# Kernel optimization log

Hardware: AMD Instinct MI355X
Metric: run time of the kernel (lower is better)

The kernel has to match this reference:

```python
import jax, jax.numpy as jnp
import numpy as np

REL_SIZE = 65
TAG_SIZE = 4


def _rope(y):
    # Interleaved rotary position embedding, matching the torch module:
    # cos_pos = cos(theta) repeat_interleave(2), sin_pos = sin(theta) repeat_interleave(2)
    # y2 = (-y1, y0, -y3, y2, ...)
    B, S, H = y.shape
    half = H // 2
    pos = jnp.arange(S, dtype=jnp.float32)[:, None]                      # (S,1)
    inv_freq = jnp.power(10000.0, -2.0 * jnp.arange(half, dtype=jnp.float32) / H)
    theta = pos * inv_freq                                               # (S, half)
    cos = jnp.repeat(jnp.cos(theta), 2, axis=-1)                          # (S, H)
    sin = jnp.repeat(jnp.sin(theta), 2, axis=-1)                          # (S, H)
    yr = y.reshape(B, S, half, 2)
    y2 = jnp.stack([-yr[..., 1], yr[..., 0]], axis=-1).reshape(B, S, H)
    return y * cos + y2 * sin


def setup_inputs() -> dict:
    key = jax.random.key(0)
    k1, k2, k3 = jax.random.split(key, 3)
    B, S, H = 1, 160, 768
    y = jax.random.normal(k1, (B, S, H), dtype=jnp.float32)
    event_idx = jax.random.randint(k2, (B, 16), 0, S)
    W1 = jax.random.normal(k3, (H, 2 * H), dtype=jnp.float32) * 0.02
    b1 = jnp.zeros((H,), dtype=jnp.float32)
    W2 = jax.random.normal(jax.random.fold_in(key, 7), (REL_SIZE * TAG_SIZE, H), dtype=jnp.float32) * 0.02
    b2 = jnp.zeros((REL_SIZE * TAG_SIZE,), dtype=jnp.float32)
    return {"y": y, "event_idx": event_idx, "W1": W1, "b1": b1, "W2": W2, "b2": b2}


def reference(y, event_idx, W1, b1, W2, b2):
    # Eval path (training=False): event_idx unused, dropout = identity, sigmoid applied.
    B, S, H = y.shape
    yrot = _rope(y)
    # Linear(cat(a, b)) is separable: split W1 into the halves acting on a and b.
    Wa, Wb = W1[:, :H], W1[:, H:]
    left = jnp.einsum('bsh,oh->bso', yrot, Wa)                  # contribution of token i (row)
    right = jnp.einsum('bsh,oh->bso', yrot, Wb) + b1            # contribution of token j (col)
    h = jax.nn.relu(left[:, :, None, :] + right[:, None, :, :])  # (B, S, S, H)
    out = jnp.einsum('bijh,oh->bijo', h, W2) + b2               # (B, S, S, 260)
    out = out.reshape(B, S, S, REL_SIZE, TAG_SIZE).transpose(0, 3, 1, 2, 4)  # (B, 65, S, S, 4)
    return jax.nn.sigmoid(out)
```

## Files before the change

### kernel.cpp

```cpp
#include <hip/hip_runtime.h>
#include <hip/hip_bf16.h>
#include <cstdint>

#define SDIM 160
#define HDIM 768
#define HALF 384
#define ODIM 260
#define OPAD 272
#define CHUNK_BYTES 34816
#define WS_SMALL 1155088
#define WS_BIG   3514384

typedef __attribute__((ext_vector_type(8))) short short8;
typedef __attribute__((ext_vector_type(4))) float floatx4;

static __device__ __forceinline__ float bf2f(unsigned short u) {
    union { unsigned int i; float f; } v; v.i = ((unsigned int)u) << 16; return v.f;
}
static __device__ __forceinline__ unsigned short f2bf(float x) {
    __hip_bfloat16 h = __float2bfloat16(x);
    return *reinterpret_cast<unsigned short*>(&h);
}
static __device__ __forceinline__ float q(float x) { return bf2f(f2bf(x)); }

__global__ __launch_bounds__(256) void prep_kernel(
    const float* __restrict__ y, const float* __restrict__ W1,
    const float* __restrict__ W2,
    unsigned short* __restrict__ yb, unsigned short* __restrict__ W2b,
    unsigned short* __restrict__ W1b) {
    int bid = blockIdx.x;
    int t = threadIdx.x;
    if (bid < SDIM) {
        int s = bid;
        for (int p = t; p < HALF; p += 256) {
            float invf = __expf(-(2.0f * (float)p / (float)HDIM) * 9.210340371976184f);
            float th = (float)s * invf;
            float c = cosf(th), sn = sinf(th);
            float y0 = y[s * HDIM + 2 * p], y1 = y[s * HDIM + 2 * p + 1];
            yb[s * HDIM + 2 * p]     = f2bf(y0 * c - y1 * sn);
            yb[s * HDIM + 2 * p + 1] = f2bf(y1 * c + y0 * sn);
        }
    } else if (bid < SDIM + 816) {
        int idx = (bid - SDIM) * 256 + t;
        int kg = idx / (OPAD * 8);
        int rem = idx - kg * (OPAD * 8);
        int row = rem >> 3, e = rem & 7;
        W2b[idx] = (row < ODIM) ? f2bf(W2[row * HDIM + kg * 8 + e])
                                : (unsigned short)0;
    } else {
        int idx = (bid - SDIM - 816) * 256 + t;
        int kg = idx / 12288;
        int rem = idx - kg * 12288;
        int row = rem >> 3, e = rem & 7;
        float v = (row < 768) ? W1[row * 1536 + kg * 8 + e]
                              : W1[(row - 768) * 1536 + 768 + kg * 8 + e];
        W1b[idx] = f2bf(v);
    }
}

__global__ __launch_bounds__(64, 2) void lr3_kernel(
    const unsigned short* __restrict__ yb, const unsigned short* __restrict__ W1b,
    const float* __restrict__ b1,
    unsigned short* __restrict__ Lb, unsigned short* __restrict__ Rb) {
    int l = threadIdx.x & 63;
    int l16 = l & 15, qd = l >> 4;
    int mtb = blockIdx.x * 4;
    int sp = blockIdx.y;
    int s0 = sp * 32 + l16;
    int s1 = s0 + 16;

    floatx4 acc[2][4];
    #pragma unroll
    for (int st = 0; st < 2; ++st)
        #pragma unroll
        for (int mtl = 0; mtl < 4; ++mtl)
            acc[st][mtl] = (floatx4){0.0f, 0.0f, 0.0f, 0.0f};

    const unsigned short* yrow0 = yb + s0 * HDIM;
    const unsigned short* yrow1 = yb + s1 * HDIM;

    for (int ks = 0; ks < 24; ++ks) {
        int k = ks * 32 + qd * 8;
        int kg = ks * 4 + qd;
        union { uint4 u; short8 s; } bu0, bu1;
        bu0.u = *reinterpret_cast<const uint4*>(yrow0 + k);
        bu1.u = *reinterpret_cast<const uint4*>(yrow1 + k);
        #pragma unroll
        for (int mtl = 0; mtl < 4; ++mtl) {
            union { uint4 u; short8 s; } au;
            au.u = *reinterpret_cast<const uint4*>(
                W1b + ((size_t)kg * 1536 + (mtb + mtl) * 16 + l16) * 8);
            acc[0][mtl] = __builtin_amdgcn_mfma_f32_16x16x32_bf16(
                au.s, bu0.s, acc[0][mtl], 0, 0, 0);
            acc[1][mtl] = __builtin_amdgcn_mfma_f32_16x16x32_bf16(
                au.s, bu1.s, acc[1][mtl], 0, 0, 0);
        }
    }

    #pragma unroll
    for (int st = 0; st < 2; ++st) {
        int s_out = sp * 32 + st * 16 + l16;
        #pragma unroll
        for (int mtl = 0; mtl < 4; ++mtl) {
            int o2 = (mtb + mtl) * 16 + qd * 4;
            unsigned short out4[4];
            if (o2 < 768) {
                #pragma unroll
                for (int r = 0; r < 4; ++r) out4[r] = f2bf(acc[st][mtl][r]);
                *reinterpret_cast<uint2*>(Lb + s_out * HDIM + o2) =
                    *reinterpret_cast<uint2*>(out4);
            } else {
                int ob = o2 - 768;
                #pragma unroll
                for (int r = 0; r < 4; ++r)
                    out4[r] = f2bf(acc[st][mtl][r] + b1[ob + r]);
                *reinterpret_cast<uint2*>(Rb + s_out * HDIM + ob) =
                    *reinterpret_cast<uint2*>(out4);
            }
        }
    }
}

__global__ __launch_bounds__(256) void lr_fallback_kernel(
    const unsigned short* __restrict__ yb, const float* __restrict__ W1,
    const float* __restrict__ b1,
    unsigned short* __restrict__ Lb, unsigned short* __restrict__ Rb) {
    int idx = blockIdx.x * 256 + threadIdx.x;
    int s = idx / 1536;
    int o2 = idx - s * 1536;
    const unsigned short* yrow = yb + s * HDIM;
    if (o2 < 768) {
        const float* wp = W1 + o2 * 1536;
        float a0 = 0.0f;
        for (int k = 0; k < HDIM; ++k) a0 += q(wp[k]) * bf2f(yrow[k]);
        Lb[s * HDIM + o2] = f2bf(a0);
    } else {
        int ob = o2 - 768;
        const float* wp = W1 + ob * 1536 + 768;
        float a0 = 0.0f;
        for (int k = 0; k < HDIM; ++k) a0 += q(wp[k]) * bf2f(yrow[k]);
        Rb[s * HDIM + ob] = f2bf(a0 + b1[ob]);
    }
}

__global__ __launch_bounds__(128, 3) void main_kernel(
    const unsigned short* __restrict__ Lb, const unsigned short* __restrict__ Rb,
    const unsigned short* __restrict__ W2b,
    const float* __restrict__ b2, float* __restrict__ out) {
    __shared__ __align__(16) unsigned char lds[CHUNK_BYTES];

    int w = threadIdx.x >> 6;
    int l = threadIdx.x & 63;
    int l16 = l & 15, qd = l >> 4;
    int mt0 = w * 9;
    int nmt = w ? 8 : 9;
    int i0 = blockIdx.x * 2;
    int j0 = blockIdx.y * 16;
    int j = j0 + l16;

    floatx4 acc[2][9];
    #pragma unroll
    for (int c = 0; c < 2; ++c)
        #pragma unroll
        for (int mtl = 0; mtl < 9; ++mtl)
            acc[c][mtl] = (floatx4){0.0f, 0.0f, 0.0f, 0.0f};

    const unsigned short* Lrow0 = Lb + i0 * HDIM;
    const unsigned short* Lrow1 = Lb + (i0 + 1) * HDIM;
    const unsigned short* Rrow  = Rb + j * HDIM;

    for (int kc = 0; kc < 12; ++kc) {
        __syncthreads();
        const uint4* gsrc = reinterpret_cast<const uint4*>(
            reinterpret_cast<const unsigned char*>(W2b) + kc * CHUNK_BYTES);
        uint4* ldsv = reinterpret_cast<uint4*>(lds);
        #pragma unroll
        for (int it = 0; it < 17; ++it) {
            int idx = it * 128 + threadIdx.x;
            ldsv[idx] = gsrc[idx];
        }
        __syncthreads();
        #pragma unroll
        for (int ks = 0; ks < 2; ++ks) {
            int k = kc * 64 + ks * 32 + qd * 8;
            short8 bfrag[2];
            #pragma unroll
            for (int c = 0; c < 2; ++c) {
                const unsigned short* Lr = c ? Lrow1 : Lrow0;
                union { uint4 u; unsigned short us[8]; } lu, ru;
                lu.u = *reinterpret_cast<const uint4*>(Lr + k);
                ru.u = *reinterpret_cast<const uint4*>(Rrow + k);
                short8 hb;
                #pragma unroll
                for (int e = 0; e < 8; ++e) {
                    float hv = bf2f(lu.us[e]) + bf2f(ru.us[e]);
                    hb[e] = (short)f2bf(fmaxf(hv, 0.0f));
                }
                bfrag[c] = hb;
            }
            int ldsbase = ((ks * 4 + qd) * OPAD + l16) * 16;
            #pragma unroll
            for (int mtl = 0; mtl < 9; ++mtl) {
                if (mtl < nmt) {
                    union { uint4 u; short8 s; } au;
                    au.u = *reinterpret_cast<const uint4*>(
                        lds + ldsbase + (mt0 + mtl) * 256);
                    acc[0][mtl] = __builtin_amdgcn_mfma_f32_16x16x32_bf16(
                        au.s, bfrag[0], acc[0][mtl], 0, 0, 0);
                    acc[1][mtl] = __builtin_amdgcn_mfma_f32_16x16x32_bf16(
                        au.s, bfrag[1], acc[1][mtl], 0, 0, 0);
                }
            }
        }
    }

    #pragma unroll
    for (int c = 0; c < 2; ++c) {
        int i = i0 + c;
        #pragma unroll
        for (int mtl = 0; mtl < 9; ++mtl) {
            if (mtl < nmt) {
                int ob = (mt0 + mtl) * 16 + qd * 4;
                if (ob < ODIM) {
                    float4 bv = *reinterpret_cast<const float4*>(b2 + ob);
                    int rel = ob >> 2;
                    float4 v;
                    v.x = 1.0f / (1.0f + __expf(-(acc[c][mtl][0] + bv.x)));
                    v.y = 1.0f / (1.0f + __expf(-(acc[c][mtl][1] + bv.y)));
                    v.z = 1.0f / (1.0f + __expf(-(acc[c][mtl][2] + bv.z)));
                    v.w = 1.0f / (1.0f + __expf(-(acc[c][mtl][3] + bv.w)));
                    *reinterpret_cast<float4*>(
                        out + (((rel * SDIM) + i) * SDIM + j) * 4) = v;
                }
            }
        }
    }
}

__global__ void ws_too_small_kernel(float* out) { out[0] = 999.0f; }

extern "C" void kernel_launch(void* const* d_in, const int* in_sizes, int n_in,
                              void* d_out, int out_size, void* d_ws, size_t ws_size,
                              hipStream_t stream) {
    const float* y  = (const float*)d_in[0];
    const float* W1 = (const float*)d_in[2];
    const float* b1 = (const float*)d_in[3];
    const float* W2 = (const float*)d_in[4];
    const float* b2 = (const float*)d_in[5];
    float* out = (float*)d_out;

    if (ws_size < (size_t)WS_SMALL) {
        ws_too_small_kernel<<<dim3(1), dim3(1), 0, stream>>>(out);
        return;
    }

    unsigned short* yb  = (unsigned short*)((char*)d_ws + 16);
    unsigned short* Lb  = yb + SDIM * HDIM;
    unsigned short* Rb  = Lb + SDIM * HDIM;
    unsigned short* W2b = Rb + SDIM * HDIM;
    unsigned short* W1b = W2b + 96 * OPAD * 8;

    if (ws_size >= (size_t)WS_BIG) {
        prep_kernel<<<dim3(SDIM + 816 + 4608), dim3(256), 0, stream>>>(
            y, W1, W2, yb, W2b, W1b);
        lr3_kernel<<<dim3(24, 5), dim3(64), 0, stream>>>(yb, W1b, b1, Lb, Rb);
        main_kernel<<<dim3(80, 10), dim3(128), 0, stream>>>(Lb, Rb, W2b, b2, out);
    } else {
        prep_kernel<<<dim3(SDIM + 816), dim3(256), 0, stream>>>(
            y, W1, W2, yb, W2b, W1b);
        lr_fallback_kernel<<<dim3(960), dim3(256), 0, stream>>>(yb, W1, b1, Lb, Rb);
        main_kernel<<<dim3(80, 10), dim3(128), 0, stream>>>(Lb, Rb, W2b, b2, out);
    }
}
```

Baseline: 130.5 us.

## Drop LDS staging of W2 and read A-fragments directly from global memory

The main kernel no longer copies W2 chunks into shared memory behind two barriers per chunk. Each wave now holds all 17 output tiles for its own 16 columns and loads W2 fragments straight from global (L2/L1-cached) memory. The grid is halved in y and occupancy hints are lowered to 2 because the accumulator count roughly doubles. This removes barrier stalls and LDS traffic, at the cost of more global load traffic per wave and higher register pressure.

Result: slower. 240.6 us (+84.3%).

```diff
diff --git a/kernel.cpp b/kernel.cpp
--- a/kernel.cpp
+++ b/kernel.cpp
@@ -7,7 +7,6 @@
 #define HALF 384
 #define ODIM 260
 #define OPAD 272
-#define CHUNK_BYTES 34816
 #define WS_SMALL 1155088
 #define WS_BIG   3514384
 
@@ -143,74 +142,54 @@
     }
 }
 
-__global__ __launch_bounds__(128, 3) void main_kernel(
+__global__ __launch_bounds__(128, 2) void main_kernel(
     const unsigned short* __restrict__ Lb, const unsigned short* __restrict__ Rb,
     const unsigned short* __restrict__ W2b,
     const float* __restrict__ b2, float* __restrict__ out) {
-    __shared__ __align__(16) unsigned char lds[CHUNK_BYTES];
-
     int w = threadIdx.x >> 6;
     int l = threadIdx.x & 63;
     int l16 = l & 15, qd = l >> 4;
-    int mt0 = w * 9;
-    int nmt = w ? 8 : 9;
     int i0 = blockIdx.x * 2;
-    int j0 = blockIdx.y * 16;
-    int j = j0 + l16;
-
-    floatx4 acc[2][9];
+    int j = blockIdx.y * 32 + w * 16 + l16;
+
+    floatx4 acc[2][17];
     #pragma unroll
     for (int c = 0; c < 2; ++c)
         #pragma unroll
-        for (int mtl = 0; mtl < 9; ++mtl)
-            acc[c][mtl] = (floatx4){0.0f, 0.0f, 0.0f, 0.0f};
+        for (int mt = 0; mt < 17; ++mt)
+            acc[c][mt] = (floatx4){0.0f, 0.0f, 0.0f, 0.0f};
 
     const unsigned short* Lrow0 = Lb + i0 * HDIM;
     const unsigned short* Lrow1 = Lb + (i0 + 1) * HDIM;
     const unsigned short* Rrow  = Rb + j * HDIM;
 
-    for (int kc = 0; kc < 12; ++kc) {
-        __syncthreads();
-        const uint4* gsrc = reinterpret_cast<const uint4*>(
-            reinterpret_cast<const unsigned char*>(W2b) + kc * CHUNK_BYTES);
-        uint4* ldsv = reinterpret_cast<uint4*>(lds);
-        #pragma unroll
-        for (int it = 0; it < 17; ++it) {
-            int idx = it * 128 + threadIdx.x;
-            ldsv[idx] = gsrc[idx];
-        }
-        __syncthreads();
-        #pragma unroll
-        for (int ks = 0; ks < 2; ++ks) {
-            int k = kc * 64 + ks * 32 + qd * 8;
-            short8 bfrag[2];
+    for (int ks = 0; ks < 24; ++ks) {
+        int k = ks * 32 + qd * 8;
+        int kg = ks * 4 + qd;
+        short8 bfrag[2];
+        #pragma unroll
+        for (int c = 0; c < 2; ++c) {
+            const unsigned short* Lr = c ? Lrow1 : Lrow0;
+            union { uint4 u; unsigned short us[8]; } lu, ru;
+            lu.u = *reinterpret_cast<const uint4*>(Lr + k);
+            ru.u = *reinterpret_cast<const uint4*>(Rrow + k);
+            short8 hb;
             #pragma unroll
-            for (int c = 0; c < 2; ++c) {
-                const unsigned short* Lr = c ? Lrow1 : Lrow0;
-                union { uint4 u; unsigned short us[8]; } lu, ru;
-                lu.u = *reinterpret_cast<const uint4*>(Lr + k);
-                ru.u = *reinterpret_cast<const uint4*>(Rrow + k);
-                short8 hb;
-                #pragma unroll
-                for (int e = 0; e < 8; ++e) {
-                    float hv = bf2f(lu.us[e]) + bf2f(ru.us[e]);
-                    hb[e] = (short)f2bf(fmaxf(hv, 0.0f));
-                }
-                bfrag[c] = hb;
+            for (int e = 0; e < 8; ++e) {
+                float hv = bf2f(lu.us[e]) + bf2f(ru.us[e]);
+                hb[e] = (short)f2bf(fmaxf(hv, 0.0f));
             }
-            int ldsbase = ((ks * 4 + qd) * OPAD + l16) * 16;
-            #pragma unroll
-            for (int mtl = 0; mtl < 9; ++mtl) {
-                if (mtl < nmt) {
-                    union { uint4 u; short8 s; } au;
-                    au.u = *reinterpret_cast<const uint4*>(
-                        lds + ldsbase + (mt0 + mtl) * 256);
-                    acc[0][mtl] = __builtin_amdgcn_mfma_f32_16x16x32_bf16(
-                        au.s, bfrag[0], acc[0][mtl], 0, 0, 0);
-                    acc[1][mtl] = __builtin_amdgcn_mfma_f32_16x16x32_bf16(
-                        au.s, bfrag[1], acc[1][mtl], 0, 0, 0);
-                }
-            }
+            bfrag[c] = hb;
+        }
+        const unsigned short* abase = W2b + (size_t)kg * OPAD * 8;
+        #pragma unroll
+        for (int mt = 0; mt < 17; ++mt) {
+            union { uint4 u; short8 s; } au;
+            au.u = *reinterpret_cast<const uint4*>(abase + (mt * 16 + l16) * 8);
+            acc[0][mt] = __builtin_amdgcn_mfma_f32_16x16x32_bf16(
+                au.s, bfrag[0], acc[0][mt], 0, 0, 0);
+            acc[1][mt] = __builtin_amdgcn_mfma_f32_16x16x32_bf16(
+                au.s, bfrag[1], acc[1][mt], 0, 0, 0);
         }
     }
 
@@ -218,20 +197,18 @@
     for (int c = 0; c < 2; ++c) {
         int i = i0 + c;
         #pragma unroll
-        for (int mtl = 0; mtl < 9; ++mtl) {
-            if (mtl < nmt) {
-                int ob = (mt0 + mtl) * 16 + qd * 4;
-                if (ob < ODIM) {
-                    float4 bv = *reinterpret_cast<const float4*>(b2 + ob);
-                    int rel = ob >> 2;
-                    float4 v;
-                    v.x = 1.0f / (1.0f + __expf(-(acc[c][mtl][0] + bv.x)));
-                    v.y = 1.0f / (1.0f + __expf(-(acc[c][mtl][1] + bv.y)));
-                    v.z = 1.0f / (1.0f + __expf(-(acc[c][mtl][2] + bv.z)));
-                    v.w = 1.0f / (1.0f + __expf(-(acc[c][mtl][3] + bv.w)));
-                    *reinterpret_cast<float4*>(
-                        out + (((rel * SDIM) + i) * SDIM + j) * 4) = v;
-                }
+        for (int mt = 0; mt < 17; ++mt) {
+            int ob = mt * 16 + qd * 4;
+            if (ob < ODIM) {
+                float4 bv = *reinterpret_cast<const float4*>(b2 + ob);
+                int rel = ob >> 2;
+                float4 v;
+                v.x = 1.0f / (1.0f + __expf(-(acc[c][mt][0] + bv.x)));
+                v.y = 1.0f / (1.0f + __expf(-(acc[c][mt][1] + bv.y)));
+                v.z = 1.0f / (1.0f + __expf(-(acc[c][mt][2] + bv.z)));
+                v.w = 1.0f / (1.0f + __expf(-(acc[c][mt][3] + bv.w)));
+                *reinterpret_cast<float4*>(
+                    out + (((rel * SDIM) + i) * SDIM + j) * 4) = v;
             }
         }
     }
@@ -264,11 +241,11 @@
         prep_kernel<<<dim3(SDIM + 816 + 4608), dim3(256), 0, stream>>>(
             y, W1, W2, yb, W2b, W1b);
         lr3_kernel<<<dim3(24, 5), dim3(64), 0, stream>>>(yb, W1b, b1, Lb, Rb);
-        main_kernel<<<dim3(80, 10), dim3(128), 0, stream>>>(Lb, Rb, W2b, b2, out);
+        main_kernel<<<dim3(80, 5), dim3(128), 0, stream>>>(Lb, Rb, W2b, b2, out);
     } else {
         prep_kernel<<<dim3(SDIM + 816), dim3(256), 0, stream>>>(
             y, W1, W2, yb, W2b, W1b);
         lr_fallback_kernel<<<dim3(960), dim3(256), 0, stream>>>(yb, W1, b1, Lb, Rb);
-        main_kernel<<<dim3(80, 10), dim3(128), 0, stream>>>(Lb, Rb, W2b, b2, out);
-    }
-}
+        main_kernel<<<dim3(80, 5), dim3(128), 0, stream>>>(Lb, Rb, W2b, b2, out);
+    }
+}
```

## Vectorize weight conversion in prep and use direct global-to-LDS loads for W2

Applied to the files above, without the earlier changes.

The prep kernel now has each thread convert eight consecutive weights using two float4 loads and one 16-byte store, instead of one element per thread, so it launches far fewer blocks. The main kernel's W2 chunk staging is replaced with the global_load_lds builtin, which copies straight from global memory into LDS without passing through registers. This is meant to cut prep launch overhead and staging register traffic. The LDS offsets are now computed per wave, which assumes each wave's 64 lanes write one contiguous 1 KB slice.

Result: faster. 127.7 us (-2.2%).

```diff
diff --git a/kernel.cpp b/kernel.cpp
--- a/kernel.cpp
+++ b/kernel.cpp
@@ -14,6 +14,9 @@
 typedef __attribute__((ext_vector_type(8))) short short8;
 typedef __attribute__((ext_vector_type(4))) float floatx4;
 
+typedef const __attribute__((address_space(1))) unsigned char gl_u8;
+typedef __attribute__((address_space(3))) unsigned char lds_u8;
+
 static __device__ __forceinline__ float bf2f(unsigned short u) {
     union { unsigned int i; float f; } v; v.i = ((unsigned int)u) << 16; return v.f;
 }
@@ -27,7 +30,7 @@
     const float* __restrict__ y, const float* __restrict__ W1,
     const float* __restrict__ W2,
     unsigned short* __restrict__ yb, unsigned short* __restrict__ W2b,
-    unsigned short* __restrict__ W1b) {
+    unsigned short* __restrict__ W1b, int do_w1b) {
     int bid = blockIdx.x;
     int t = threadIdx.x;
     if (bid < SDIM) {
@@ -40,21 +43,35 @@
             yb[s * HDIM + 2 * p]     = f2bf(y0 * c - y1 * sn);
             yb[s * HDIM + 2 * p + 1] = f2bf(y1 * c + y0 * sn);
         }
-    } else if (bid < SDIM + 816) {
+    } else if (bid < SDIM + 102) {
         int idx = (bid - SDIM) * 256 + t;
-        int kg = idx / (OPAD * 8);
-        int rem = idx - kg * (OPAD * 8);
-        int row = rem >> 3, e = rem & 7;
-        W2b[idx] = (row < ODIM) ? f2bf(W2[row * HDIM + kg * 8 + e])
-                                : (unsigned short)0;
-    } else {
-        int idx = (bid - SDIM - 816) * 256 + t;
-        int kg = idx / 12288;
-        int rem = idx - kg * 12288;
-        int row = rem >> 3, e = rem & 7;
-        float v = (row < 768) ? W1[row * 1536 + kg * 8 + e]
-                              : W1[(row - 768) * 1536 + 768 + kg * 8 + e];
-        W1b[idx] = f2bf(v);
+        if (idx < 96 * OPAD) {
+            int kg = idx % 96, row = idx / 96;
+            unsigned short o8[8];
+            if (row < ODIM) {
+                float4 a = *reinterpret_cast<const float4*>(W2 + row * HDIM + kg * 8);
+                float4 b = *reinterpret_cast<const float4*>(W2 + row * HDIM + kg * 8 + 4);
+                o8[0] = f2bf(a.x); o8[1] = f2bf(a.y); o8[2] = f2bf(a.z); o8[3] = f2bf(a.w);
+                o8[4] = f2bf(b.x); o8[5] = f2bf(b.y); o8[6] = f2bf(b.z); o8[7] = f2bf(b.w);
+            } else {
+                #pragma unroll
+                for (int e = 0; e < 8; ++e) o8[e] = 0;
+            }
+            *reinterpret_cast<uint4*>(W2b + ((size_t)kg * OPAD + row) * 8) =
+                *reinterpret_cast<uint4*>(o8);
+        }
+    } else if (do_w1b) {
+        int idx = (bid - SDIM - 102) * 256 + t;
+        int kg = idx % 96, row = idx / 96;
+        const float* src = (row < 768) ? (W1 + row * 1536 + kg * 8)
+                                       : (W1 + (row - 768) * 1536 + 768 + kg * 8);
+        float4 a = *reinterpret_cast<const float4*>(src);
+        float4 b = *reinterpret_cast<const float4*>(src + 4);
+        unsigned short o8[8];
+        o8[0] = f2bf(a.x); o8[1] = f2bf(a.y); o8[2] = f2bf(a.z); o8[3] = f2bf(a.w);
+        o8[4] = f2bf(b.x); o8[5] = f2bf(b.y); o8[6] = f2bf(b.z); o8[7] = f2bf(b.w);
+        *reinterpret_cast<uint4*>(W1b + ((size_t)kg * 1536 + row) * 8) =
+            *reinterpret_cast<uint4*>(o8);
     }
 }
 
@@ -171,13 +188,15 @@
 
     for (int kc = 0; kc < 12; ++kc) {
         __syncthreads();
-        const uint4* gsrc = reinterpret_cast<const uint4*>(
-            reinterpret_cast<const unsigned char*>(W2b) + kc * CHUNK_BYTES);
-        uint4* ldsv = reinterpret_cast<uint4*>(lds);
+        const unsigned char* gsrc =
+            reinterpret_cast<const unsigned char*>(W2b) + kc * CHUNK_BYTES;
         #pragma unroll
         for (int it = 0; it < 17; ++it) {
-            int idx = it * 128 + threadIdx.x;
-            ldsv[idx] = gsrc[idx];
+            int off = (w * 17 + it) * 1024;
+            __builtin_amdgcn_global_load_lds(
+                (gl_u8*)(gsrc + off + l * 16),
+                (lds_u8*)(lds + off),
+                16, 0, 0);
         }
         __syncthreads();
         #pragma unroll
@@ -261,13 +280,13 @@
     unsigned short* W1b = W2b + 96 * OPAD * 8;
 
     if (ws_size >= (size_t)WS_BIG) {
-        prep_kernel<<<dim3(SDIM + 816 + 4608), dim3(256), 0, stream>>>(
-            y, W1, W2, yb, W2b, W1b);
+        prep_kernel<<<dim3(SDIM + 102 + 576), dim3(256), 0, stream>>>(
+            y, W1, W2, yb, W2b, W1b, 1);
         lr3_kernel<<<dim3(24, 5), dim3(64), 0, stream>>>(yb, W1b, b1, Lb, Rb);
         main_kernel<<<dim3(80, 10), dim3(128), 0, stream>>>(Lb, Rb, W2b, b2, out);
     } else {
-        prep_kernel<<<dim3(SDIM + 816), dim3(256), 0, stream>>>(
-            y, W1, W2, yb, W2b, W1b);
+        prep_kernel<<<dim3(SDIM + 102), dim3(256), 0, stream>>>(
+            y, W1, W2, yb, W2b, W1b, 0);
         lr_fallback_kernel<<<dim3(960), dim3(256), 0, stream>>>(yb, W1, b1, Lb, Rb);
         main_kernel<<<dim3(80, 10), dim3(128), 0, stream>>>(Lb, Rb, W2b, b2, out);
     }
```
